# Kernel optimization log

Measured on AMD Instinct MI355X. Metric: run time of the kernel, lower is better.

## Reference

```python
import jax, jax.numpy as jnp
import numpy as np

B, N, D, H, DD = 4, 256, 768, 12, 64
HD = D // H  # head_dim = 64
SCALE = float(np.sqrt(HD))


def _layernorm(x, g, b, eps=1e-5):
    mu = jnp.mean(x, axis=-1, keepdims=True)
    var = jnp.var(x, axis=-1, keepdims=True)
    return (x - mu) / jnp.sqrt(var + eps) * g + b


def setup_inputs() -> dict:
    key = jax.random.key(0)
    ks = jax.random.split(key, 20)
    def w(k, shape, fan_in):
        return (jax.random.normal(k, shape, jnp.float32) / np.sqrt(fan_in)).astype(jnp.float32)
    x = jax.random.normal(ks[0], (B, N, D), jnp.float32)
    dist = jax.random.normal(ks[1], (B, N, N, DD), jnp.float32)
    mask = jax.random.randint(ks[2], (B, N, N), 0, 2) > 0
    eye = jnp.eye(N, dtype=bool)[None]
    edge_mask = jnp.logical_or(mask, eye)  # guarantee no fully-masked row
    return {
        'x': x, 'distance_features': dist, 'edge_mask': edge_mask,
        'qkv_w': w(ks[3], (D, 3 * D), D), 'qkv_b': jnp.zeros((3 * D,), jnp.float32),
        'out_w': w(ks[4], (D, D), D), 'out_b': jnp.zeros((D,), jnp.float32),
        'rb_w1': w(ks[5], (DD, D), DD), 'rb_b1': jnp.zeros((D,), jnp.float32),
        'rb_w2': w(ks[6], (D, H), D), 'rb_b2': jnp.zeros((H,), jnp.float32),
        'gate_w1': w(ks[7], (D, D), D), 'gate_b1': jnp.zeros((D,), jnp.float32),
        'gate_w2': w(ks[8], (D, D), D), 'gate_b2': jnp.zeros((D,), jnp.float32),
        'ff_w1': w(ks[9], (D, 2 * D), D), 'ff_b1': jnp.zeros((2 * D,), jnp.float32),
        'ff_w2': w(ks[10], (2 * D, D), 2 * D), 'ff_b2': jnp.zeros((D,), jnp.float32),
        'ln1_g': jnp.ones((D,), jnp.float32), 'ln1_b': jnp.zeros((D,), jnp.float32),
        'ln2_g': jnp.ones((D,), jnp.float32), 'ln2_b': jnp.zeros((D,), jnp.float32),
    }


def reference(x, distance_features, edge_mask, qkv_w, qkv_b, out_w, out_b,
              rb_w1, rb_b1, rb_w2, rb_b2, gate_w1, gate_b1, gate_w2, gate_b2,
              ff_w1, ff_b1, ff_w2, ff_b2, ln1_g, ln1_b, ln2_g, ln2_b):
    residual = x
    xn = _layernorm(x, ln1_g, ln1_b)
    qkv = xn @ qkv_w + qkv_b
    q, k, v = jnp.split(qkv, 3, axis=-1)
    q = q.reshape(B, N, H, HD)
    k = k.reshape(B, N, H, HD)
    v = v.reshape(B, N, H, HD)
    logits = jnp.einsum('bihd,bjhd->bhij', q, k) / SCALE
    bias = jax.nn.silu(distance_features @ rb_w1 + rb_b1) @ rb_w2 + rb_b2  # [B,N,N,H]
    logits = logits + jnp.transpose(bias, (0, 3, 1, 2))
    neg = jnp.finfo(logits.dtype).min
    logits = jnp.where(edge_mask[:, None, :, :], logits, neg)
    attn = jax.nn.softmax(logits, axis=-1)
    context = jnp.einsum('bhij,bjhd->bihd', attn, v).reshape(B, N, D)
    gated = jax.nn.silu(xn @ gate_w1 + gate_b1) @ gate_w2 + gate_b2
    x2 = residual + (context * jax.nn.sigmoid(gated)) @ out_w + out_b
    y = _layernorm(x2, ln2_g, ln2_b)
    ff = jax.nn.gelu(y @ ff_w1 + ff_b1, approximate=False) @ ff_w2 + ff_b2
    return x2 + ff
```

## Files before the change

kernel.cpp:

```cpp
#include <hip/hip_runtime.h>
#include <hip/hip_bf16.h>
#include <cmath>

#define U16 unsigned short

typedef __bf16 bf16x8_t __attribute__((ext_vector_type(8)));
typedef float f32x4_t __attribute__((ext_vector_type(4)));

union Frag { uint4 u4; unsigned u[4]; bf16x8_t b8; U16 s[8]; };

__device__ __forceinline__ float b2f(U16 u) {
  union { unsigned int i; float f; } x; x.i = ((unsigned int)u) << 16; return x.f;
}
__device__ __forceinline__ U16 f2b(float f) {
  union { float f; unsigned int i; } x; x.f = f;
  unsigned int r = x.i + 0x7FFFu + ((x.i >> 16) & 1u);
  return (U16)(r >> 16);
}
__device__ __forceinline__ unsigned cvt_pk_bf16(float a, float b) {
  union { __hip_bfloat162 h2; unsigned u; } x;
  x.h2 = __float22bfloat162_rn(make_float2(a, b));
  return x.u;
}
__device__ __forceinline__ float fast_silu(float z) {
  return z * __builtin_amdgcn_rcpf(1.f + __expf(-z));
}
__device__ __forceinline__ void load_lds16(const U16* g, U16* l) {
  __builtin_amdgcn_global_load_lds((const __attribute__((address_space(1))) void*)g,
                                   (__attribute__((address_space(3))) void*)l, 16, 0, 0);
}

__global__ __launch_bounds__(256) void prep_kernel(
    const float* __restrict__ qkv_w, const float* __restrict__ out_w,
    const float* __restrict__ g1w, const float* __restrict__ g2w,
    const float* __restrict__ ff1w, const float* __restrict__ ff2w,
    const float* __restrict__ rb1w, const float* __restrict__ rb2w,
    const float* __restrict__ qkv_b, const float* __restrict__ gate_b1,
    U16* __restrict__ qkv_wT, U16* __restrict__ out_wT, U16* __restrict__ g1wT,
    U16* __restrict__ g2wT, U16* __restrict__ ff1wT, U16* __restrict__ ff2wT,
    U16* __restrict__ rb1wT, U16* __restrict__ rb2wL, float* __restrict__ qg_bias) {
  int bid = blockIdx.x;
  if (bid >= 5856) {
    int idx = (bid - 5856) * 256 + threadIdx.x;
    qg_bias[idx] = (idx < 2304) ? qkv_b[idx] : gate_b1[idx - 2304];
    return;
  }
  if (bid >= 5808) {
    int idx = (bid - 5808) * 256 + threadIdx.x;
    int j = idx & 7, lane = (idx >> 3) & 63, pp = idx >> 9;
    int row = lane & 15, col = pp * 32 + ((lane >> 4) << 3) + j;
    rb2wL[idx] = (row < 12) ? f2b(rb2w[col * 12 + row]) : (U16)0;
    return;
  }
  const float* in; U16* out; int R, C, base;
  if (bid < 1728)      { in = qkv_w; out = qkv_wT; R = 768;  C = 2304; base = 0; }
  else if (bid < 2304) { in = out_w; out = out_wT; R = 768;  C = 768;  base = 1728; }
  else if (bid < 2880) { in = g1w;   out = g1wT;   R = 768;  C = 768;  base = 2304; }
  else if (bid < 3456) { in = g2w;   out = g2wT;   R = 768;  C = 768;  base = 2880; }
  else if (bid < 4608) { in = ff1w;  out = ff1wT;  R = 768;  C = 1536; base = 3456; }
  else if (bid < 5760) { in = ff2w;  out = ff2wT;  R = 1536; C = 768;  base = 4608; }
  else                 { in = rb1w;  out = rb1wT;  R = 64;   C = 768;  base = 5760; }
  int bx = bid - base, tilesx = C / 32;
  int c0 = (bx % tilesx) * 32, r0 = (bx / tilesx) * 32;
  __shared__ float tile[32][33];
  int tx = threadIdx.x & 31, ty = threadIdx.x >> 5;
#pragma unroll
  for (int yy = 0; yy < 4; ++yy)
    tile[ty + yy * 8][tx] = in[(size_t)(r0 + ty + yy * 8) * C + c0 + tx];
  __syncthreads();
#pragma unroll
  for (int yy = 0; yy < 4; ++yy)
    out[(size_t)(c0 + ty + yy * 8) * R + r0 + tx] = f2b(tile[tx][ty + yy * 8]);
}

__global__ __launch_bounds__(256) void kt_kernel(const float* __restrict__ qkvb,
                                                 float* __restrict__ kT) {
  int bid = blockIdx.x;
  int bh = bid >> 4, tile = bid & 15;
  int b = bh / 12, h = bh % 12;
  int n0 = (tile & 7) * 32, d0 = (tile >> 3) * 32;
  __shared__ float t[32][33];
  int tx = threadIdx.x & 31, ty = threadIdx.x >> 5;
#pragma unroll
  for (int yy = 0; yy < 4; ++yy)
    t[ty + yy * 8][tx] =
        qkvb[(size_t)(b * 256 + n0 + ty + yy * 8) * 2304 + 768 + h * 64 + d0 + tx];
  __syncthreads();
#pragma unroll
  for (int yy = 0; yy < 4; ++yy)
    kT[(size_t)bh * 16384 + (size_t)(d0 + ty + yy * 8) * 256 + n0 + tx] = t[tx][ty + yy * 8];
}

__global__ __launch_bounds__(256) void ln_kernel(const float* __restrict__ X,
                                                 const float* __restrict__ gam,
                                                 const float* __restrict__ bet,
                                                 U16* __restrict__ Y) {
  int row = blockIdx.x, tid = threadIdx.x, lane = tid & 63, wave = tid >> 6;
  __shared__ float p1[4], p2[4];
  float v[3];
#pragma unroll
  for (int j = 0; j < 3; ++j) v[j] = X[(size_t)row * 768 + tid + j * 256];
  float s1 = v[0] + v[1] + v[2];
  float s2 = v[0] * v[0] + v[1] * v[1] + v[2] * v[2];
#pragma unroll
  for (int m = 32; m > 0; m >>= 1) {
    s1 += __shfl_xor(s1, m);
    s2 += __shfl_xor(s2, m);
  }
  if (lane == 0) { p1[wave] = s1; p2[wave] = s2; }
  __syncthreads();
  float t1 = p1[0] + p1[1] + p1[2] + p1[3];
  float t2 = p2[0] + p2[1] + p2[2] + p2[3];
  float mean = t1 * (1.f / 768.f);
  float var = t2 * (1.f / 768.f) - mean * mean;
  float rstd = rsqrtf(var + 1e-5f);
#pragma unroll
  for (int j = 0; j < 3; ++j) {
    int c = tid + j * 256;
    Y[(size_t)row * 768 + c] = f2b((v[j] - mean) * rstd * gam[c] + bet[c]);
  }
}

template <int EPI, bool OUTF32>
__global__ __launch_bounds__(256) void gemm_bt(const U16* __restrict__ A,
                                               const U16* __restrict__ BT,
                                               const float* __restrict__ bias,
                                               const float* __restrict__ other,
                                               void* __restrict__ Cout,
                                               float* __restrict__ Cout2,
                                               int M, int N, int K) {
  __shared__ __align__(16) U16 sA[64 * 32];
  __shared__ __align__(16) U16 sB[64 * 32];
  int tid = threadIdx.x;
  int lane = tid & 63, wave = tid >> 6;
  int m0 = blockIdx.y * 64, n0 = blockIdx.x * 64;
  int wm = (wave >> 1) * 32, wn = (wave & 1) * 32;
  int lm = lane & 15, lq = lane >> 4;
  int srow = tid >> 2, scol = (tid & 3) * 8;
  const U16* ag = A + (size_t)(m0 + srow) * K + scol;
  const U16* bg = BT + (size_t)(n0 + srow) * K + scol;
  U16* lA = &sA[tid * 8];
  U16* lB = &sB[tid * 8];
  f32x4_t acc[2][2] = {};
  for (int k0 = 0; k0 < K; k0 += 32) {
    __syncthreads();
    load_lds16(ag + k0, lA);
    load_lds16(bg + k0, lB);
    __syncthreads();
    Frag af[2], bf[2];
#pragma unroll
    for (int mt = 0; mt < 2; ++mt)
      af[mt].u4 = *(const uint4*)&sA[(wm + mt * 16 + lm) * 32 + lq * 8];
#pragma unroll
    for (int nt = 0; nt < 2; ++nt)
      bf[nt].u4 = *(const uint4*)&sB[(wn + nt * 16 + lm) * 32 + lq * 8];
#pragma unroll
    for (int mt = 0; mt < 2; ++mt)
#pragma unroll
      for (int nt = 0; nt < 2; ++nt)
        acc[mt][nt] = __builtin_amdgcn_mfma_f32_16x16x32_bf16(af[mt].b8, bf[nt].b8,
                                                              acc[mt][nt], 0, 0, 0);
  }
#pragma unroll
  for (int nt = 0; nt < 2; ++nt) {
    int gc = n0 + wn + nt * 16 + lm;
    float bz = bias[gc];
#pragma unroll
    for (int mt = 0; mt < 2; ++mt) {
#pragma unroll
      for (int r = 0; r < 4; ++r) {
        int gr = m0 + wm + mt * 16 + lq * 4 + r;
        float z = acc[mt][nt][r] + bz;
        if (EPI == 5) {
          if (gc < 2304) Cout2[(size_t)gr * 2304 + gc] = z;
          else ((U16*)Cout)[(size_t)gr * 768 + gc - 2304] = f2b(fast_silu(z));
          continue;
        }
        size_t idx = (size_t)gr * N + gc;
        float o;
        if (EPI == 0) o = z;
        else if (EPI == 1) o = fast_silu(z);
        else if (EPI == 2) o = 0.5f * z * (1.f + erff(z * 0.70710678118f));
        else if (EPI == 3) o = other[idx] * __builtin_amdgcn_rcpf(1.f + __expf(-z));
        else o = z + other[idx];
        if (OUTF32) ((float*)Cout)[idx] = o;
        else ((U16*)Cout)[idx] = f2b(o);
      }
    }
  }
}

__global__ __launch_bounds__(256) void rb_kernel(const float* __restrict__ dist,
                                                 const U16* __restrict__ w1T,
                                                 const float* __restrict__ b1,
                                                 const U16* __restrict__ w2L,
                                                 const float* __restrict__ b2,
                                                 float* __restrict__ biasOut) {
  int tid = threadIdx.x;
  int lane = tid & 63, wave = tid >> 6;
  int lm = lane & 15, lq = lane >> 4;
  int r0 = blockIdx.x * 256;
  float hb = (lm < 12) ? b2[lm] : 0.f;
  Frag bd[4][2];
#pragma unroll
  for (int g = 0; g < 4; ++g) {
    const float* ap = dist + (size_t)(r0 + (wave * 4 + g) * 16 + lm) * 64 + lq * 8;
    float4 v0 = ((const float4*)ap)[0];
    float4 v1 = ((const float4*)ap)[1];
    float4 v2 = ((const float4*)(ap + 32))[0];
    float4 v3 = ((const float4*)(ap + 32))[1];
    bd[g][0].u[0] = cvt_pk_bf16(v0.x, v0.y); bd[g][0].u[1] = cvt_pk_bf16(v0.z, v0.w);
    bd[g][0].u[2] = cvt_pk_bf16(v1.x, v1.y); bd[g][0].u[3] = cvt_pk_bf16(v1.z, v1.w);
    bd[g][1].u[0] = cvt_pk_bf16(v2.x, v2.y); bd[g][1].u[1] = cvt_pk_bf16(v2.z, v2.w);
    bd[g][1].u[2] = cvt_pk_bf16(v3.x, v3.y); bd[g][1].u[3] = cvt_pk_bf16(v3.z, v3.w);
  }
  const U16* w1p0 = w1T + (size_t)(((lm >> 2) << 3) + (lm & 3)) * 64 + lq * 8;
  const U16* w1p1 = w1p0 + 4 * 64;
  const U16* w2p = w2L + lane * 8;
  const float* b1p = b1 + lq * 8;
  Frag cw00, cw01, cw10, cw11, cwb;
  cw00.u4 = *(const uint4*)w1p0;
  cw01.u4 = *(const uint4*)(w1p0 + 32);
  cw10.u4 = *(const uint4*)w1p1;
  cw11.u4 = *(const uint4*)(w1p1 + 32);
  cwb.u4 = *(const uint4*)w2p;
  float4 cb0 = *(const float4*)b1p;
  float4 cb1 = *(const float4*)(b1p + 4);
  f32x4_t bacc[4] = {{hb, hb, hb, hb}, {hb, hb, hb, hb}, {hb, hb, hb, hb}, {hb, hb, hb, hb}};
  for (int pp = 0; pp < 24; ++pp) {
    Frag nw00 = cw00, nw01 = cw01, nw10 = cw10, nw11 = cw11, nwb = cwb;
    float4 nb0 = cb0, nb1 = cb1;
    if (pp < 23) {
      w1p0 += 32 * 64; w1p1 += 32 * 64; w2p += 64 * 8; b1p += 32;
      nw00.u4 = *(const uint4*)w1p0;
      nw01.u4 = *(const uint4*)(w1p0 + 32);
      nw10.u4 = *(const uint4*)w1p1;
      nw11.u4 = *(const uint4*)(w1p1 + 32);
      nwb.u4 = *(const uint4*)w2p;
      nb0 = *(const float4*)b1p;
      nb1 = *(const float4*)(b1p + 4);
    }
    f32x4_t cz0 = {cb0.x, cb0.y, cb0.z, cb0.w};
    f32x4_t cz1 = {cb1.x, cb1.y, cb1.z, cb1.w};
#pragma unroll
    for (int g = 0; g < 4; ++g) {
      f32x4_t z0 = cz0, z1 = cz1;
      z0 = __builtin_amdgcn_mfma_f32_16x16x32_bf16(cw00.b8, bd[g][0].b8, z0, 0, 0, 0);
      z0 = __builtin_amdgcn_mfma_f32_16x16x32_bf16(cw01.b8, bd[g][1].b8, z0, 0, 0, 0);
      z1 = __builtin_amdgcn_mfma_f32_16x16x32_bf16(cw10.b8, bd[g][0].b8, z1, 0, 0, 0);
      z1 = __builtin_amdgcn_mfma_f32_16x16x32_bf16(cw11.b8, bd[g][1].b8, z1, 0, 0, 0);
      float s0 = fast_silu(z0[0]), s1 = fast_silu(z0[1]);
      float s2 = fast_silu(z0[2]), s3 = fast_silu(z0[3]);
      float t0 = fast_silu(z1[0]), t1 = fast_silu(z1[1]);
      float t2 = fast_silu(z1[2]), t3 = fast_silu(z1[3]);
      Frag af2;
      af2.u[0] = cvt_pk_bf16(s0, s1); af2.u[1] = cvt_pk_bf16(s2, s3);
      af2.u[2] = cvt_pk_bf16(t0, t1); af2.u[3] = cvt_pk_bf16(t2, t3);
      bacc[g] = __builtin_amdgcn_mfma_f32_16x16x32_bf16(af2.b8, cwb.b8, bacc[g], 0, 0, 0);
    }
    cw00 = nw00; cw01 = nw01; cw10 = nw10; cw11 = nw11; cwb = nwb;
    cb0 = nb0; cb1 = nb1;
  }
  if (lm < 12) {
#pragma unroll
    for (int g = 0; g < 4; ++g) {
#pragma unroll
      for (int r = 0; r < 4; ++r) {
        int gr = r0 + (wave * 4 + g) * 16 + lq * 4 + r;
        int b = gr >> 16, rem = gr & 65535, i = rem >> 8, j = rem & 255;
        biasOut[(((size_t)b * 12 + lm) * 256 + i) * 256 + j] = bacc[g][r];
      }
    }
  }
}

__global__ __launch_bounds__(256) void attn_kernel(const float* __restrict__ qkv,
                                                   const float* __restrict__ kT,
                                                   const float* __restrict__ biasB,
                                                   const int* __restrict__ mask,
                                                   float* __restrict__ ctx) {
  int tid = threadIdx.x, lane = tid & 63, w = tid >> 6;
  int bh = blockIdx.y, b = bh / 12, h = bh % 12;
  int i0 = blockIdx.x * 16;
  __shared__ float sQ[16][66];
  __shared__ float sP[4][4][256];
  {
    int r = tid >> 4, c = (tid & 15) * 4;
    *(float4*)&sQ[r][c] =
        *(const float4*)&qkv[((size_t)(b * 256 + i0 + r)) * 2304 + h * 64 + c];
  }
  int iw = i0 + w * 4;
  float lacc[4][4] = {};
  const float* kp = kT + (size_t)bh * 16384 + lane;
#pragma unroll 4
  for (int d = 0; d < 64; d += 2) {
    float k00 = kp[d * 256], k01 = kp[d * 256 + 64];
    float k02 = kp[d * 256 + 128], k03 = kp[d * 256 + 192];
    float k10 = kp[d * 256 + 256], k11 = kp[d * 256 + 320];
    float k12 = kp[d * 256 + 384], k13 = kp[d * 256 + 448];
#pragma unroll
    for (int qi = 0; qi < 4; ++qi) {
      float2 q2 = *(const float2*)&sQ[w * 4 + qi][d];
      lacc[qi][0] += q2.x * k00 + q2.y * k10;
      lacc[qi][1] += q2.x * k01 + q2.y * k11;
      lacc[qi][2] += q2.x * k02 + q2.y * k12;
      lacc[qi][3] += q2.x * k03 + q2.y * k13;
    }
  }
#pragma unroll
  for (int qi = 0; qi < 4; ++qi) {
    int gi = iw + qi;
    const float* brow = biasB + (((size_t)b * 12 + h) * 256 + gi) * 256;
    const int* mrow = mask + ((size_t)b * 256 + gi) * 256;
    float lg[4];
#pragma unroll
    for (int jc = 0; jc < 4; ++jc) {
      float lv = lacc[qi][jc] * 0.125f + brow[jc * 64 + lane];
      lg[jc] = mrow[jc * 64 + lane] ? lv : -1e30f;
    }
    float mx = fmaxf(fmaxf(lg[0], lg[1]), fmaxf(lg[2], lg[3]));
#pragma unroll
    for (int m = 32; m > 0; m >>= 1) mx = fmaxf(mx, __shfl_xor(mx, m));
    float e[4], sum = 0.f;
#pragma unroll
    for (int jc = 0; jc < 4; ++jc) { e[jc] = __expf(lg[jc] - mx); sum += e[jc]; }
#pragma unroll
    for (int m = 32; m > 0; m >>= 1) sum += __shfl_xor(sum, m);
    float inv = __builtin_amdgcn_rcpf(sum);
#pragma unroll
    for (int jc = 0; jc < 4; ++jc) sP[w][qi][jc * 64 + lane] = e[jc] * inv;
  }
  float ca[4] = {0.f, 0.f, 0.f, 0.f};
  const float* vcol = qkv + (size_t)b * 256 * 2304 + 1536 + h * 64 + lane;
#pragma unroll 2
  for (int j4 = 0; j4 < 256; j4 += 4) {
    float4 p0 = *(const float4*)&sP[w][0][j4];
    float4 p1 = *(const float4*)&sP[w][1][j4];
    float4 p2 = *(const float4*)&sP[w][2][j4];
    float4 p3 = *(const float4*)&sP[w][3][j4];
    const float* pp0 = (const float*)&p0;
    const float* pp1 = (const float*)&p1;
    const float* pp2 = (const float*)&p2;
    const float* pp3 = (const float*)&p3;
#pragma unroll
    for (int jj = 0; jj < 4; ++jj) {
      float v = vcol[(size_t)(j4 + jj) * 2304];
      ca[0] += pp0[jj] * v;
      ca[1] += pp1[jj] * v;
      ca[2] += pp2[jj] * v;
      ca[3] += pp3[jj] * v;
    }
  }
#pragma unroll
  for (int qi = 0; qi < 4; ++qi)
    ctx[((size_t)(b * 256 + iw + qi)) * 768 + h * 64 + lane] = ca[qi];
}

extern "C" void kernel_launch(void* const* d_in, const int* in_sizes, int n_in,
                              void* d_out, int out_size, void* d_ws, size_t ws_size,
                              hipStream_t stream) {
  const float* x       = (const float*)d_in[0];
  const float* dist    = (const float*)d_in[1];
  const int* mask      = (const int*)d_in[2];
  const float* qkv_w   = (const float*)d_in[3];
  const float* qkv_b   = (const float*)d_in[4];
  const float* out_w   = (const float*)d_in[5];
  const float* out_b   = (const float*)d_in[6];
  const float* rb_w1   = (const float*)d_in[7];
  const float* rb_b1   = (const float*)d_in[8];
  const float* rb_w2   = (const float*)d_in[9];
  const float* rb_b2   = (const float*)d_in[10];
  const float* gate_w1 = (const float*)d_in[11];
  const float* gate_b1 = (const float*)d_in[12];
  const float* gate_w2 = (const float*)d_in[13];
  const float* gate_b2 = (const float*)d_in[14];
  const float* ff_w1   = (const float*)d_in[15];
  const float* ff_b1   = (const float*)d_in[16];
  const float* ff_w2   = (const float*)d_in[17];
  const float* ff_b2   = (const float*)d_in[18];
  const float* ln1_g   = (const float*)d_in[19];
  const float* ln1_b   = (const float*)d_in[20];
  const float* ln2_g   = (const float*)d_in[21];
  const float* ln2_b   = (const float*)d_in[22];

  char* w = (char*)d_ws;
  auto alloc = [&](size_t bytes) {
    char* p = w;
    w += (bytes + 255) & ~(size_t)255;
    return p;
  };
  U16* xn      = (U16*)alloc(1024 * 768 * 2);
  float* qkvb  = (float*)alloc((size_t)1024 * 2304 * 4);
  float* kT    = (float*)alloc((size_t)48 * 64 * 256 * 4);
  U16* qg_wT   = (U16*)alloc((size_t)3072 * 768 * 2);
  U16* qkv_wT  = qg_wT;
  U16* g1wT    = qg_wT + (size_t)2304 * 768;
  float* qg_b  = (float*)alloc(3072 * 4);
  U16* out_wT  = (U16*)alloc(768 * 768 * 2);
  U16* g2wT    = (U16*)alloc(768 * 768 * 2);
  U16* ff1wT   = (U16*)alloc(1536 * 768 * 2);
  U16* ff2wT   = (U16*)alloc(768 * 1536 * 2);
  U16* rb1wT   = (U16*)alloc(768 * 64 * 2);
  U16* rb2wL   = (U16*)alloc(24 * 64 * 8 * 2);
  float* biasB = (float*)alloc((size_t)4 * 12 * 256 * 256 * 4);
  float* ctx   = (float*)alloc(1024 * 768 * 4);
  U16* g1      = (U16*)alloc(1024 * 768 * 2);
  U16* cg      = (U16*)alloc(1024 * 768 * 2);
  float* x2    = (float*)alloc(1024 * 768 * 4);
  U16* y       = (U16*)alloc(1024 * 768 * 2);
  U16* f1      = (U16*)alloc(1024 * 1536 * 2);
  (void)ws_size; (void)in_sizes; (void)n_in; (void)out_size;

  prep_kernel<<<5868, 256, 0, stream>>>(qkv_w, out_w, gate_w1, gate_w2, ff_w1, ff_w2,
                                        rb_w1, rb_w2, qkv_b, gate_b1,
                                        qkv_wT, out_wT, g1wT, g2wT, ff1wT, ff2wT,
                                        rb1wT, rb2wL, qg_b);

  ln_kernel<<<1024, 256, 0, stream>>>(x, ln1_g, ln1_b, xn);
  gemm_bt<5, false><<<dim3(48, 16), 256, 0, stream>>>(xn, qg_wT, qg_b, nullptr, g1,
                                                      qkvb, 1024, 3072, 768);
  kt_kernel<<<768, 256, 0, stream>>>(qkvb, kT);
  rb_kernel<<<1024, 256, 0, stream>>>(dist, rb1wT, rb_b1, rb2wL, rb_b2, biasB);
  attn_kernel<<<dim3(16, 48), 256, 0, stream>>>(qkvb, kT, biasB, mask, ctx);
  gemm_bt<3, false><<<dim3(12, 16), 256, 0, stream>>>(g1, g2wT, gate_b2, ctx, cg,
                                                      nullptr, 1024, 768, 768);
  gemm_bt<4, true><<<dim3(12, 16), 256, 0, stream>>>(cg, out_wT, out_b, x, x2,
                                                     nullptr, 1024, 768, 768);
  ln_kernel<<<1024, 256, 0, stream>>>(x2, ln2_g, ln2_b, y);
  gemm_bt<2, false><<<dim3(24, 16), 256, 0, stream>>>(y, ff1wT, ff_b1, nullptr, f1,
                                                      nullptr, 1024, 1536, 768);
  gemm_bt<4, true><<<dim3(12, 16), 256, 0, stream>>>(f1, ff2wT, ff_b2, x2, (float*)d_out,
                                                     nullptr, 1024, 768, 1536);
}
```

Measured before the change: 327.6 us.

## Fuse LN1 into prep, merge QKV GEMM with rel-bias, double-buffer GEMMs, drop kT

LayerNorm1 now runs as extra blocks of the weight-prep kernel, and the QKV/gate GEMM and the relative-bias MLP run as one launch with blocks split by index. The separate K-transpose kernel is removed: attention loads K into LDS as bf16 inside each block. GEMMs gain double-buffered LDS tiles so the next k-slice loads while the current one computes, and the rb loop is restructured into an even/odd prefetch. Together these cut launches and serial gaps between stages. In exchange, attention now rebuilds K per block with strided global reads, and K is rounded to bf16, which loses some precision.

Result: no change. 327.2 us (-0.1%).

```diff
diff --git a/kernel.cpp b/kernel.cpp
--- a/kernel.cpp
+++ b/kernel.cpp
@@ -28,6 +28,36 @@
 __device__ __forceinline__ void load_lds16(const U16* g, U16* l) {
   __builtin_amdgcn_global_load_lds((const __attribute__((address_space(1))) void*)g,
                                    (__attribute__((address_space(3))) void*)l, 16, 0, 0);
+}
+
+__device__ __forceinline__ void ln_row(int row, const float* __restrict__ X,
+                                       const float* __restrict__ gam,
+                                       const float* __restrict__ bet,
+                                       U16* __restrict__ Y) {
+  int tid = threadIdx.x, lane = tid & 63, wave = tid >> 6;
+  __shared__ float p1[4], p2[4];
+  float v[3];
+#pragma unroll
+  for (int j = 0; j < 3; ++j) v[j] = X[(size_t)row * 768 + tid + j * 256];
+  float s1 = v[0] + v[1] + v[2];
+  float s2 = v[0] * v[0] + v[1] * v[1] + v[2] * v[2];
+#pragma unroll
+  for (int m = 32; m > 0; m >>= 1) {
+    s1 += __shfl_xor(s1, m);
+    s2 += __shfl_xor(s2, m);
+  }
+  if (lane == 0) { p1[wave] = s1; p2[wave] = s2; }
+  __syncthreads();
+  float t1 = p1[0] + p1[1] + p1[2] + p1[3];
+  float t2 = p2[0] + p2[1] + p2[2] + p2[3];
+  float mean = t1 * (1.f / 768.f);
+  float var = t2 * (1.f / 768.f) - mean * mean;
+  float rstd = rsqrtf(var + 1e-5f);
+#pragma unroll
+  for (int j = 0; j < 3; ++j) {
+    int c = tid + j * 256;
+    Y[(size_t)row * 768 + c] = f2b((v[j] - mean) * rstd * gam[c] + bet[c]);
+  }
 }
 
 __global__ __launch_bounds__(256) void prep_kernel(
@@ -38,8 +68,14 @@
     const float* __restrict__ qkv_b, const float* __restrict__ gate_b1,
     U16* __restrict__ qkv_wT, U16* __restrict__ out_wT, U16* __restrict__ g1wT,
     U16* __restrict__ g2wT, U16* __restrict__ ff1wT, U16* __restrict__ ff2wT,
-    U16* __restrict__ rb1wT, U16* __restrict__ rb2wL, float* __restrict__ qg_bias) {
+    U16* __restrict__ rb1wT, U16* __restrict__ rb2wL, float* __restrict__ qg_bias,
+    const float* __restrict__ x, const float* __restrict__ ln1_g,
+    const float* __restrict__ ln1_b, U16* __restrict__ xn) {
   int bid = blockIdx.x;
+  if (bid >= 5868) {
+    ln_row(bid - 5868, x, ln1_g, ln1_b, xn);
+    return;
+  }
   if (bid >= 5856) {
     int idx = (bid - 5856) * 256 + threadIdx.x;
     qg_bias[idx] = (idx < 2304) ? qkv_b[idx] : gate_b1[idx - 2304];
@@ -73,87 +109,41 @@
     out[(size_t)(c0 + ty + yy * 8) * R + r0 + tx] = f2b(tile[tx][ty + yy * 8]);
 }
 
-__global__ __launch_bounds__(256) void kt_kernel(const float* __restrict__ qkvb,
-                                                 float* __restrict__ kT) {
-  int bid = blockIdx.x;
-  int bh = bid >> 4, tile = bid & 15;
-  int b = bh / 12, h = bh % 12;
-  int n0 = (tile & 7) * 32, d0 = (tile >> 3) * 32;
-  __shared__ float t[32][33];
-  int tx = threadIdx.x & 31, ty = threadIdx.x >> 5;
-#pragma unroll
-  for (int yy = 0; yy < 4; ++yy)
-    t[ty + yy * 8][tx] =
-        qkvb[(size_t)(b * 256 + n0 + ty + yy * 8) * 2304 + 768 + h * 64 + d0 + tx];
-  __syncthreads();
-#pragma unroll
-  for (int yy = 0; yy < 4; ++yy)
-    kT[(size_t)bh * 16384 + (size_t)(d0 + ty + yy * 8) * 256 + n0 + tx] = t[tx][ty + yy * 8];
-}
-
-__global__ __launch_bounds__(256) void ln_kernel(const float* __restrict__ X,
-                                                 const float* __restrict__ gam,
-                                                 const float* __restrict__ bet,
-                                                 U16* __restrict__ Y) {
-  int row = blockIdx.x, tid = threadIdx.x, lane = tid & 63, wave = tid >> 6;
-  __shared__ float p1[4], p2[4];
-  float v[3];
-#pragma unroll
-  for (int j = 0; j < 3; ++j) v[j] = X[(size_t)row * 768 + tid + j * 256];
-  float s1 = v[0] + v[1] + v[2];
-  float s2 = v[0] * v[0] + v[1] * v[1] + v[2] * v[2];
-#pragma unroll
-  for (int m = 32; m > 0; m >>= 1) {
-    s1 += __shfl_xor(s1, m);
-    s2 += __shfl_xor(s2, m);
-  }
-  if (lane == 0) { p1[wave] = s1; p2[wave] = s2; }
-  __syncthreads();
-  float t1 = p1[0] + p1[1] + p1[2] + p1[3];
-  float t2 = p2[0] + p2[1] + p2[2] + p2[3];
-  float mean = t1 * (1.f / 768.f);
-  float var = t2 * (1.f / 768.f) - mean * mean;
-  float rstd = rsqrtf(var + 1e-5f);
-#pragma unroll
-  for (int j = 0; j < 3; ++j) {
-    int c = tid + j * 256;
-    Y[(size_t)row * 768 + c] = f2b((v[j] - mean) * rstd * gam[c] + bet[c]);
-  }
-}
-
 template <int EPI, bool OUTF32>
-__global__ __launch_bounds__(256) void gemm_bt(const U16* __restrict__ A,
-                                               const U16* __restrict__ BT,
-                                               const float* __restrict__ bias,
-                                               const float* __restrict__ other,
-                                               void* __restrict__ Cout,
-                                               float* __restrict__ Cout2,
-                                               int M, int N, int K) {
-  __shared__ __align__(16) U16 sA[64 * 32];
-  __shared__ __align__(16) U16 sB[64 * 32];
+__device__ __forceinline__ void gemm_core(U16* sA, U16* sB,
+                                          const U16* __restrict__ A,
+                                          const U16* __restrict__ BT,
+                                          const float* __restrict__ bias,
+                                          const float* __restrict__ other,
+                                          void* __restrict__ Cout,
+                                          float* __restrict__ Cout2,
+                                          int N, int K, int bx, int by) {
   int tid = threadIdx.x;
   int lane = tid & 63, wave = tid >> 6;
-  int m0 = blockIdx.y * 64, n0 = blockIdx.x * 64;
+  int m0 = by * 64, n0 = bx * 64;
   int wm = (wave >> 1) * 32, wn = (wave & 1) * 32;
   int lm = lane & 15, lq = lane >> 4;
   int srow = tid >> 2, scol = (tid & 3) * 8;
   const U16* ag = A + (size_t)(m0 + srow) * K + scol;
   const U16* bg = BT + (size_t)(n0 + srow) * K + scol;
-  U16* lA = &sA[tid * 8];
-  U16* lB = &sB[tid * 8];
+  int nit = K >> 5;
+  load_lds16(ag, sA + tid * 8);
+  load_lds16(bg, sB + tid * 8);
   f32x4_t acc[2][2] = {};
-  for (int k0 = 0; k0 < K; k0 += 32) {
+  for (int i = 0; i < nit; ++i) {
     __syncthreads();
-    load_lds16(ag + k0, lA);
-    load_lds16(bg + k0, lB);
-    __syncthreads();
+    int cb = (i & 1) * 2048, nb = ((i + 1) & 1) * 2048;
+    if (i + 1 < nit) {
+      load_lds16(ag + (i + 1) * 32, sA + nb + tid * 8);
+      load_lds16(bg + (i + 1) * 32, sB + nb + tid * 8);
+    }
     Frag af[2], bf[2];
 #pragma unroll
     for (int mt = 0; mt < 2; ++mt)
-      af[mt].u4 = *(const uint4*)&sA[(wm + mt * 16 + lm) * 32 + lq * 8];
+      af[mt].u4 = *(const uint4*)&sA[cb + (wm + mt * 16 + lm) * 32 + lq * 8];
 #pragma unroll
     for (int nt = 0; nt < 2; ++nt)
-      bf[nt].u4 = *(const uint4*)&sB[(wn + nt * 16 + lm) * 32 + lq * 8];
+      bf[nt].u4 = *(const uint4*)&sB[cb + (wn + nt * 16 + lm) * 32 + lq * 8];
 #pragma unroll
     for (int mt = 0; mt < 2; ++mt)
 #pragma unroll
@@ -190,16 +180,27 @@
   }
 }
 
-__global__ __launch_bounds__(256) void rb_kernel(const float* __restrict__ dist,
-                                                 const U16* __restrict__ w1T,
-                                                 const float* __restrict__ b1,
-                                                 const U16* __restrict__ w2L,
-                                                 const float* __restrict__ b2,
-                                                 float* __restrict__ biasOut) {
+template <int EPI, bool OUTF32>
+__global__ __launch_bounds__(256) void gemm_bt(const U16* __restrict__ A,
+                                               const U16* __restrict__ BT,
+                                               const float* __restrict__ bias,
+                                               const float* __restrict__ other,
+                                               void* __restrict__ Cout,
+                                               int N, int K) {
+  __shared__ __align__(16) U16 sA[2 * 2048];
+  __shared__ __align__(16) U16 sB[2 * 2048];
+  gemm_core<EPI, OUTF32>(sA, sB, A, BT, bias, other, Cout, nullptr, N, K,
+                         blockIdx.x, blockIdx.y);
+}
+
+__device__ void rb_body(int bid, const float* __restrict__ dist,
+                        const U16* __restrict__ w1T, const float* __restrict__ b1,
+                        const U16* __restrict__ w2L, const float* __restrict__ b2,
+                        float* __restrict__ biasOut) {
   int tid = threadIdx.x;
   int lane = tid & 63, wave = tid >> 6;
   int lm = lane & 15, lq = lane >> 4;
-  int r0 = blockIdx.x * 256;
+  int r0 = bid * 256;
   float hb = (lm < 12) ? b2[lm] : 0.f;
   Frag bd[4][2];
 #pragma unroll
@@ -215,40 +216,34 @@
     bd[g][1].u[2] = cvt_pk_bf16(v3.x, v3.y); bd[g][1].u[3] = cvt_pk_bf16(v3.z, v3.w);
   }
   const U16* w1p0 = w1T + (size_t)(((lm >> 2) << 3) + (lm & 3)) * 64 + lq * 8;
-  const U16* w1p1 = w1p0 + 4 * 64;
+  const U16* w1p1 = w1p0 + 256;
   const U16* w2p = w2L + lane * 8;
   const float* b1p = b1 + lq * 8;
-  Frag cw00, cw01, cw10, cw11, cwb;
-  cw00.u4 = *(const uint4*)w1p0;
-  cw01.u4 = *(const uint4*)(w1p0 + 32);
-  cw10.u4 = *(const uint4*)w1p1;
-  cw11.u4 = *(const uint4*)(w1p1 + 32);
-  cwb.u4 = *(const uint4*)w2p;
-  float4 cb0 = *(const float4*)b1p;
-  float4 cb1 = *(const float4*)(b1p + 4);
   f32x4_t bacc[4] = {{hb, hb, hb, hb}, {hb, hb, hb, hb}, {hb, hb, hb, hb}, {hb, hb, hb, hb}};
-  for (int pp = 0; pp < 24; ++pp) {
-    Frag nw00 = cw00, nw01 = cw01, nw10 = cw10, nw11 = cw11, nwb = cwb;
-    float4 nb0 = cb0, nb1 = cb1;
-    if (pp < 23) {
-      w1p0 += 32 * 64; w1p1 += 32 * 64; w2p += 64 * 8; b1p += 32;
-      nw00.u4 = *(const uint4*)w1p0;
-      nw01.u4 = *(const uint4*)(w1p0 + 32);
-      nw10.u4 = *(const uint4*)w1p1;
-      nw11.u4 = *(const uint4*)(w1p1 + 32);
-      nwb.u4 = *(const uint4*)w2p;
-      nb0 = *(const float4*)b1p;
-      nb1 = *(const float4*)(b1p + 4);
-    }
-    f32x4_t cz0 = {cb0.x, cb0.y, cb0.z, cb0.w};
-    f32x4_t cz1 = {cb1.x, cb1.y, cb1.z, cb1.w};
+
+  auto loadw = [&](int j, Frag& f00, Frag& f01, Frag& f10, Frag& f11, Frag& fwb,
+                   float4& fb0, float4& fb1) {
+    const U16* p0 = w1p0 + (size_t)j * 2048;
+    const U16* p1 = w1p1 + (size_t)j * 2048;
+    f00.u4 = *(const uint4*)p0;
+    f01.u4 = *(const uint4*)(p0 + 32);
+    f10.u4 = *(const uint4*)p1;
+    f11.u4 = *(const uint4*)(p1 + 32);
+    fwb.u4 = *(const uint4*)(w2p + (size_t)j * 512);
+    fb0 = *(const float4*)(b1p + j * 32);
+    fb1 = *(const float4*)(b1p + j * 32 + 4);
+  };
+  auto comp = [&](Frag& f00, Frag& f01, Frag& f10, Frag& f11, Frag& fwb,
+                  float4 fb0, float4 fb1) {
+    f32x4_t cz0 = {fb0.x, fb0.y, fb0.z, fb0.w};
+    f32x4_t cz1 = {fb1.x, fb1.y, fb1.z, fb1.w};
 #pragma unroll
     for (int g = 0; g < 4; ++g) {
       f32x4_t z0 = cz0, z1 = cz1;
-      z0 = __builtin_amdgcn_mfma_f32_16x16x32_bf16(cw00.b8, bd[g][0].b8, z0, 0, 0, 0);
-      z0 = __builtin_amdgcn_mfma_f32_16x16x32_bf16(cw01.b8, bd[g][1].b8, z0, 0, 0, 0);
-      z1 = __builtin_amdgcn_mfma_f32_16x16x32_bf16(cw10.b8, bd[g][0].b8, z1, 0, 0, 0);
-      z1 = __builtin_amdgcn_mfma_f32_16x16x32_bf16(cw11.b8, bd[g][1].b8, z1, 0, 0, 0);
+      z0 = __builtin_amdgcn_mfma_f32_16x16x32_bf16(f00.b8, bd[g][0].b8, z0, 0, 0, 0);
+      z0 = __builtin_amdgcn_mfma_f32_16x16x32_bf16(f01.b8, bd[g][1].b8, z0, 0, 0, 0);
+      z1 = __builtin_amdgcn_mfma_f32_16x16x32_bf16(f10.b8, bd[g][0].b8, z1, 0, 0, 0);
+      z1 = __builtin_amdgcn_mfma_f32_16x16x32_bf16(f11.b8, bd[g][1].b8, z1, 0, 0, 0);
       float s0 = fast_silu(z0[0]), s1 = fast_silu(z0[1]);
       float s2 = fast_silu(z0[2]), s3 = fast_silu(z0[3]);
       float t0 = fast_silu(z1[0]), t1 = fast_silu(z1[1]);
@@ -256,10 +251,18 @@
       Frag af2;
       af2.u[0] = cvt_pk_bf16(s0, s1); af2.u[1] = cvt_pk_bf16(s2, s3);
       af2.u[2] = cvt_pk_bf16(t0, t1); af2.u[3] = cvt_pk_bf16(t2, t3);
-      bacc[g] = __builtin_amdgcn_mfma_f32_16x16x32_bf16(af2.b8, cwb.b8, bacc[g], 0, 0, 0);
-    }
-    cw00 = nw00; cw01 = nw01; cw10 = nw10; cw11 = nw11; cwb = nwb;
-    cb0 = nb0; cb1 = nb1;
+      bacc[g] = __builtin_amdgcn_mfma_f32_16x16x32_bf16(af2.b8, fwb.b8, bacc[g], 0, 0, 0);
+    }
+  };
+
+  Frag e00, e01, e10, e11, ewb, o00, o01, o10, o11, owb;
+  float4 eb0, eb1, ob0, ob1;
+  loadw(0, e00, e01, e10, e11, ewb, eb0, eb1);
+  for (int pp = 0; pp < 24; pp += 2) {
+    loadw(pp + 1, o00, o01, o10, o11, owb, ob0, ob1);
+    comp(e00, e01, e10, e11, ewb, eb0, eb1);
+    if (pp + 2 < 24) loadw(pp + 2, e00, e01, e10, e11, ewb, eb0, eb1);
+    comp(o00, o01, o10, o11, owb, ob0, ob1);
   }
   if (lm < 12) {
 #pragma unroll
@@ -274,14 +277,31 @@
   }
 }
 
+__global__ __launch_bounds__(256) void qkvrb_kernel(
+    const U16* __restrict__ xn, const U16* __restrict__ qg_wT,
+    const float* __restrict__ qg_b, float* __restrict__ qkvb, U16* __restrict__ g1,
+    const float* __restrict__ dist, const U16* __restrict__ rb1wT,
+    const float* __restrict__ rb_b1, const U16* __restrict__ rb2wL,
+    const float* __restrict__ rb_b2, float* __restrict__ biasB) {
+  __shared__ __align__(16) U16 sA[2 * 2048];
+  __shared__ __align__(16) U16 sB[2 * 2048];
+  int bid = blockIdx.x;
+  if (bid < 768) {
+    gemm_core<5, false>(sA, sB, xn, qg_wT, qg_b, nullptr, g1, qkvb, 3072, 768,
+                        bid % 48, bid / 48);
+  } else {
+    rb_body(bid - 768, dist, rb1wT, rb_b1, rb2wL, rb_b2, biasB);
+  }
+}
+
 __global__ __launch_bounds__(256) void attn_kernel(const float* __restrict__ qkv,
-                                                   const float* __restrict__ kT,
                                                    const float* __restrict__ biasB,
                                                    const int* __restrict__ mask,
                                                    float* __restrict__ ctx) {
   int tid = threadIdx.x, lane = tid & 63, w = tid >> 6;
   int bh = blockIdx.y, b = bh / 12, h = bh % 12;
   int i0 = blockIdx.x * 16;
+  __shared__ U16 sK[64 * 258];
   __shared__ float sQ[16][66];
   __shared__ float sP[4][4][256];
   {
@@ -289,22 +309,30 @@
     *(float4*)&sQ[r][c] =
         *(const float4*)&qkv[((size_t)(b * 256 + i0 + r)) * 2304 + h * 64 + c];
   }
+  {
+    const float* kr = qkv + ((size_t)(b * 256 + w * 64)) * 2304 + 768 + h * 64 + lane;
+#pragma unroll 8
+    for (int rr = 0; rr < 64; ++rr) {
+      float kv = kr[(size_t)rr * 2304];
+      sK[lane * 258 + w * 64 + rr] = (U16)cvt_pk_bf16(kv, kv);
+    }
+  }
+  __syncthreads();
   int iw = i0 + w * 4;
   float lacc[4][4] = {};
-  const float* kp = kT + (size_t)bh * 16384 + lane;
 #pragma unroll 4
-  for (int d = 0; d < 64; d += 2) {
-    float k00 = kp[d * 256], k01 = kp[d * 256 + 64];
-    float k02 = kp[d * 256 + 128], k03 = kp[d * 256 + 192];
-    float k10 = kp[d * 256 + 256], k11 = kp[d * 256 + 320];
-    float k12 = kp[d * 256 + 384], k13 = kp[d * 256 + 448];
+  for (int d = 0; d < 64; ++d) {
+    float k0 = b2f(sK[d * 258 + lane]);
+    float k1 = b2f(sK[d * 258 + 64 + lane]);
+    float k2 = b2f(sK[d * 258 + 128 + lane]);
+    float k3 = b2f(sK[d * 258 + 192 + lane]);
 #pragma unroll
     for (int qi = 0; qi < 4; ++qi) {
-      float2 q2 = *(const float2*)&sQ[w * 4 + qi][d];
-      lacc[qi][0] += q2.x * k00 + q2.y * k10;
-      lacc[qi][1] += q2.x * k01 + q2.y * k11;
-      lacc[qi][2] += q2.x * k02 + q2.y * k12;
-      lacc[qi][3] += q2.x * k03 + q2.y * k13;
+      float qv = sQ[w * 4 + qi][d];
+      lacc[qi][0] += qv * k0;
+      lacc[qi][1] += qv * k1;
+      lacc[qi][2] += qv * k2;
+      lacc[qi][3] += qv * k3;
     }
   }
 #pragma unroll
@@ -354,6 +382,13 @@
 #pragma unroll
   for (int qi = 0; qi < 4; ++qi)
     ctx[((size_t)(b * 256 + iw + qi)) * 768 + h * 64 + lane] = ca[qi];
+}
+
+__global__ __launch_bounds__(256) void ln_kernel(const float* __restrict__ X,
+                                                 const float* __restrict__ gam,
+                                                 const float* __restrict__ bet,
+                                                 U16* __restrict__ Y) {
+  ln_row(blockIdx.x, X, gam, bet, Y);
 }
 
 extern "C" void kernel_launch(void* const* d_in, const int* in_sizes, int n_in,
@@ -391,7 +426,6 @@
   };
   U16* xn      = (U16*)alloc(1024 * 768 * 2);
   float* qkvb  = (float*)alloc((size_t)1024 * 2304 * 4);
-  float* kT    = (float*)alloc((size_t)48 * 64 * 256 * 4);
   U16* qg_wT   = (U16*)alloc((size_t)3072 * 768 * 2);
   U16* qkv_wT  = qg_wT;
   U16* g1wT    = qg_wT + (size_t)2304 * 768;
@@ -411,24 +445,20 @@
   U16* f1      = (U16*)alloc(1024 * 1536 * 2);
   (void)ws_size; (void)in_sizes; (void)n_in; (void)out_size;
 
-  prep_kernel<<<5868, 256, 0, stream>>>(qkv_w, out_w, gate_w1, gate_w2, ff_w1, ff_w2,
+  prep_kernel<<<6892, 256, 0, stream>>>(qkv_w, out_w, gate_w1, gate_w2, ff_w1, ff_w2,
                                         rb_w1, rb_w2, qkv_b, gate_b1,
                                         qkv_wT, out_wT, g1wT, g2wT, ff1wT, ff2wT,
-                                        rb1wT, rb2wL, qg_b);
-
-  ln_kernel<<<1024, 256, 0, stream>>>(x, ln1_g, ln1_b, xn);
-  gemm_bt<5, false><<<dim3(48, 16), 256, 0, stream>>>(xn, qg_wT, qg_b, nullptr, g1,
-                                                      qkvb, 1024, 3072, 768);
-  kt_kernel<<<768, 256, 0, stream>>>(qkvb, kT);
-  rb_kernel<<<1024, 256, 0, stream>>>(dist, rb1wT, rb_b1, rb2wL, rb_b2, biasB);
-  attn_kernel<<<dim3(16, 48), 256, 0, stream>>>(qkvb, kT, biasB, mask, ctx);
+                                        rb1wT, rb2wL, qg_b, x, ln1_g, ln1_b, xn);
+  qkvrb_kernel<<<1792, 256, 0, stream>>>(xn, qg_wT, qg_b, qkvb, g1,
+                                         dist, rb1wT, rb_b1, rb2wL, rb_b2, biasB);
+  attn_kernel<<<dim3(16, 48), 256, 0, stream>>>(qkvb, biasB, mask, ctx);
   gemm_bt<3, false><<<dim3(12, 16), 256, 0, stream>>>(g1, g2wT, gate_b2, ctx, cg,
-                                                      nullptr, 1024, 768, 768);
+                                                      768, 768);
   gemm_bt<4, true><<<dim3(12, 16), 256, 0, stream>>>(cg, out_wT, out_b, x, x2,
-                                                     nullptr, 1024, 768, 768);
+                                                     768, 768);
   ln_kernel<<<1024, 256, 0, stream>>>(x2, ln2_g, ln2_b, y);
   gemm_bt<2, false><<<dim3(24, 16), 256, 0, stream>>>(y, ff1wT, ff_b1, nullptr, f1,
-                                                      nullptr, 1024, 1536, 768);
+                                                      1536, 768);
   gemm_bt<4, true><<<dim3(12, 16), 256, 0, stream>>>(f1, ff2wT, ff_b2, x2, (float*)d_out,
-                                                     nullptr, 1024, 768, 1536);
-}
+                                                     768, 1536);
+}
```
